# Performance work log

Measured on AMD Instinct MI355X. Metric: run time of the kernel, lower is better.

## Reference

```python
import jax, jax.numpy as jnp
import numpy as np

B, C, H, W = 4, 256, 64, 64
DQK = C // 8  # 32
EPS = 1e-5

def conv1x1(x, Wt, b):
    # 1x1 conv == per-pixel channel matmul. x: [B,C,H,W], Wt: [O,C], b: [O]
    return jnp.einsum('bchw,oc->bohw', x, Wt) + b[None, :, None, None]

def setup_inputs() -> dict:
    key = jax.random.key(0)
    ks = jax.random.split(key, 4)
    s = 1.0 / np.sqrt(C)
    return {
        'x': jax.random.normal(ks[0], (B, C, H, W), dtype=jnp.float32),
        'Wq': jax.random.normal(ks[1], (DQK, C), dtype=jnp.float32) * s,
        'bq': jnp.zeros((DQK,), dtype=jnp.float32),
        'Wk': jax.random.normal(ks[2], (DQK, C), dtype=jnp.float32) * s,
        'bk': jnp.zeros((DQK,), dtype=jnp.float32),
        'Wv': jax.random.normal(ks[3], (C, C), dtype=jnp.float32) * s,
        'bv': jnp.zeros((C,), dtype=jnp.float32),
        'bn_gamma': jnp.ones((C,), dtype=jnp.float32),
        'bn_beta': jnp.zeros((C,), dtype=jnp.float32),
    }

def reference(x, Wq, bq, Wk, bk, Wv, bv, bn_gamma, bn_beta):
    b, c, h, w = x.shape
    n = h * w
    q = conv1x1(x, Wq, bq).reshape(b, -1, n)   # [B, C/8, N]
    k = conv1x1(x, Wk, bk).reshape(b, -1, n)   # [B, C/8, N]
    v = conv1x1(x, Wv, bv).reshape(b, -1, n)   # [B, C,   N]
    # attention_weights = softmax(Q^T K) over last dim (no 1/sqrt(d) scaling)
    attn = jax.nn.softmax(jnp.einsum('bdi,bdj->bij', q, k), axis=-1)  # [B,N,N]
    out = jnp.einsum('bci,bij->bcj', v, attn).reshape(b, c, h, w)
    # BatchNorm2d (training mode: batch stats over B,H,W, biased var)
    mean = jnp.mean(out, axis=(0, 2, 3), keepdims=True)
    var = jnp.var(out, axis=(0, 2, 3), keepdims=True)
    out = (out - mean) * jax.lax.rsqrt(var + EPS)
    out = out * bn_gamma[None, :, None, None] + bn_beta[None, :, None, None]
    return x + out * 1e-05
```

## Files before the change

### kernel.cpp

```cpp
#include <hip/hip_runtime.h>
#include <hip/hip_bf16.h>

#define NB 4
#define NC 256
#define NN 4096

typedef __bf16 bf16x8 __attribute__((ext_vector_type(8)));
typedef float f32x4 __attribute__((ext_vector_type(4)));
typedef unsigned short u16x4 __attribute__((ext_vector_type(4)));
typedef unsigned short u16x8 __attribute__((ext_vector_type(8)));
typedef unsigned int u32x4 __attribute__((ext_vector_type(4)));

__device__ __forceinline__ unsigned short f2bf(float f) {
  union { float f; unsigned u; } v; v.f = f;
  unsigned r = v.u + 0x7fffu + ((v.u >> 16) & 1u);
  return (unsigned short)(r >> 16);
}
__device__ __forceinline__ float bf2f(unsigned short h) {
  union { unsigned u; float f; } v; v.u = ((unsigned)h) << 16;
  return v.f;
}

__global__ __launch_bounds__(256) void k0_prep(const float* __restrict__ Wq,
                                               const float* __restrict__ Wk,
                                               const float* __restrict__ Wv,
                                               unsigned short* __restrict__ Wcat,
                                               unsigned short* __restrict__ Wvb,
                                               float* __restrict__ stats) {
  int tid = blockIdx.x * 256 + threadIdx.x;
  int nt = gridDim.x * 256;
  for (int i = tid; i < 64 * NC; i += nt) {
    int d = i >> 8, c = i & 255;
    float v = (d < 32) ? Wq[d * NC + c] : Wk[(d - 32) * NC + c];
    Wcat[i] = f2bf(v);
  }
  for (int i = tid; i < NC * NC; i += nt) Wvb[i] = f2bf(Wv[i]);
  for (int i = tid; i < 1024; i += nt) stats[i] = 0.f;
}

__global__ __launch_bounds__(256) void k1_cvt_tr(const float* __restrict__ x,
                                                 unsigned short* __restrict__ xbf,
                                                 unsigned short* __restrict__ xT) {
  __shared__ __align__(16) unsigned short lt[64][68];
  int bid = blockIdx.x;
  int b  = bid >> 8;
  int cb = (bid >> 6) & 3;
  int nb = bid & 63;
  int c0 = cb * 64, n0 = nb * 64;
  int t = threadIdx.x;
  int tc = t >> 4;
  int tn = (t & 15) * 4;
#pragma unroll
  for (int it = 0; it < 4; ++it) {
    int c = c0 + tc + it * 16;
    f32x4 xv = *reinterpret_cast<const f32x4*>(&x[((size_t)b * NC + c) * NN + n0 + tn]);
    u16x4 hv;
    hv[0] = f2bf(xv[0]); hv[1] = f2bf(xv[1]); hv[2] = f2bf(xv[2]); hv[3] = f2bf(xv[3]);
    *reinterpret_cast<u16x4*>(&xbf[((size_t)b * NC + c) * NN + n0 + tn]) = hv;
    *reinterpret_cast<u16x4*>(&lt[tc + it * 16][tn]) = hv;
  }
  __syncthreads();
  int nl = t >> 2;
  int cl0 = (t & 3) * 16;
  u16x8 o0, o1;
#pragma unroll
  for (int q = 0; q < 8; ++q) o0[q] = lt[cl0 + q][nl];
#pragma unroll
  for (int q = 0; q < 8; ++q) o1[q] = lt[cl0 + 8 + q][nl];
  size_t ro = ((size_t)b * NN + n0 + nl) * NC + c0 + cl0;
  *reinterpret_cast<u16x8*>(&xT[ro]) = o0;
  *reinterpret_cast<u16x8*>(&xT[ro + 8]) = o1;
}

__global__ __launch_bounds__(256, 2) void k2_qk(const unsigned short* __restrict__ xT,
                                                const unsigned short* __restrict__ Wcat,
                                                const float* __restrict__ bq,
                                                const float* __restrict__ bk,
                                                unsigned short* __restrict__ Qt,
                                                unsigned short* __restrict__ Kt) {
  __shared__ __align__(16) unsigned short lt2[64][72];
  int bid = blockIdx.x;
  int b = bid >> 6, it = bid & 63;
  int i0 = it * 64;
  int t = threadIdx.x;
  int w = t >> 6, l = t & 63, l15 = l & 15, g = l >> 4;

  f32x4 acc[4];
#pragma unroll
  for (int f = 0; f < 4; ++f) acc[f] = f32x4{0.f, 0.f, 0.f, 0.f};

  const unsigned short* xrow = &xT[((size_t)b * NN + i0 + w * 16 + l15) * NC];
#pragma unroll
  for (int ks = 0; ks < 8; ++ks) {
    bf16x8 a = *reinterpret_cast<const bf16x8*>(&xrow[ks * 32 + g * 8]);
#pragma unroll
    for (int f = 0; f < 4; ++f) {
      bf16x8 bb = *reinterpret_cast<const bf16x8*>(&Wcat[(f * 16 + l15) * NC + ks * 32 + g * 8]);
      acc[f] = __builtin_amdgcn_mfma_f32_16x16x32_bf16(a, bb, acc[f], 0, 0, 0);
    }
  }
#pragma unroll
  for (int f = 0; f < 4; ++f) {
    int d = f * 16 + l15;
    float bias = (f < 2) ? bq[d] : bk[d - 32];
#pragma unroll
    for (int r = 0; r < 4; ++r)
      lt2[w * 16 + g * 4 + r][d] = f2bf(acc[f][r] + bias);
  }
  __syncthreads();
  int il = t >> 2, quad = t & 3;
  u32x4 v0 = *reinterpret_cast<const u32x4*>(&lt2[il][quad * 16]);
  u32x4 v1 = *reinterpret_cast<const u32x4*>(&lt2[il][quad * 16 + 8]);
  unsigned short* dst = (quad < 2) ? &Qt[((size_t)b * NN + i0 + il) * 32 + quad * 16]
                                   : &Kt[((size_t)b * NN + i0 + il) * 32 + (quad - 2) * 16];
  *reinterpret_cast<u32x4*>(dst) = v0;
  *reinterpret_cast<u32x4*>(&dst[8]) = v1;
}

__global__ __launch_bounds__(256, 4) void k3_rowsum(const unsigned short* __restrict__ Qt,
                                                    const unsigned short* __restrict__ Kt,
                                                    float* __restrict__ invD) {
  __shared__ float sred[4][16];
  int bid = blockIdx.x;
  int b = bid >> 8, it = bid & 255;
  int i0 = it * 16;
  int t = threadIdx.x, w = t >> 6, l = t & 63, l15 = l & 15, g = l >> 4;
  bf16x8 a = *reinterpret_cast<const bf16x8*>(&Qt[((size_t)b * NN + i0 + l15) * 32 + g * 8]);
  float rs0 = 0.f, rs1 = 0.f, rs2 = 0.f, rs3 = 0.f;
  int jbase = w * 1024;
  for (int jc = 0; jc < 16; ++jc) {
    int jb = jbase + jc * 64;
#pragma unroll
    for (int f = 0; f < 4; ++f) {
      bf16x8 bb = *reinterpret_cast<const bf16x8*>(&Kt[((size_t)b * NN + jb + f * 16 + l15) * 32 + g * 8]);
      f32x4 s = __builtin_amdgcn_mfma_f32_16x16x32_bf16(a, bb, f32x4{0.f, 0.f, 0.f, 0.f}, 0, 0, 0);
      rs0 += __expf(s[0]); rs1 += __expf(s[1]); rs2 += __expf(s[2]); rs3 += __expf(s[3]);
    }
  }
#pragma unroll
  for (int m = 1; m < 16; m <<= 1) {
    rs0 += __shfl_xor(rs0, m); rs1 += __shfl_xor(rs1, m);
    rs2 += __shfl_xor(rs2, m); rs3 += __shfl_xor(rs3, m);
  }
  if (l15 == 0) {
    sred[w][g * 4 + 0] = rs0; sred[w][g * 4 + 1] = rs1;
    sred[w][g * 4 + 2] = rs2; sred[w][g * 4 + 3] = rs3;
  }
  __syncthreads();
  if (t < 16) {
    float d = sred[0][t] + sred[1][t] + sred[2][t] + sred[3][t];
    invD[(size_t)b * NN + i0 + t] = 1.0f / d;
  }
}

__global__ __launch_bounds__(256, 2) void k4_attn(const unsigned short* __restrict__ xbf,
                                                  const unsigned short* __restrict__ Qt,
                                                  const unsigned short* __restrict__ Kt,
                                                  const float* __restrict__ invD,
                                                  unsigned short* __restrict__ TtL,
                                                  unsigned short* __restrict__ TtH,
                                                  float* __restrict__ sLo,
                                                  float* __restrict__ sHi) {
  __shared__ __align__(16) unsigned short plt[4096];
  __shared__ float sArr[4][64];
  int bid = blockIdx.x;
  int b = bid >> 7, ih = (bid >> 6) & 1, jt = bid & 63;
  int j0 = jt * 64;
  int t = threadIdx.x, w = t >> 6, l = t & 63, l15 = l & 15, g = l >> 4;
  unsigned short* Tt = ih ? TtH : TtL;
  float* scol = ih ? sHi : sLo;

  bf16x8 bkf[4];
#pragma unroll
  for (int f = 0; f < 4; ++f)
    bkf[f] = *reinterpret_cast<const bf16x8*>(&Kt[((size_t)b * NN + j0 + f * 16 + l15) * 32 + g * 8]);

  f32x4 acc[4][4];
#pragma unroll
  for (int ci = 0; ci < 4; ++ci)
#pragma unroll
    for (int f = 0; f < 4; ++f) acc[ci][f] = f32x4{0.f, 0.f, 0.f, 0.f};
  float scs[4] = {0.f, 0.f, 0.f, 0.f};

  for (int ic = 0; ic < 32; ++ic) {
    int ibase = (ih * 32 + ic) * 64;
    bf16x8 aq = *reinterpret_cast<const bf16x8*>(&Qt[((size_t)b * NN + ibase + w * 16 + l15) * 32 + g * 8]);
    f32x4 inv4 = *reinterpret_cast<const f32x4*>(&invD[(size_t)b * NN + ibase + w * 16 + g * 4]);
#pragma unroll
    for (int f = 0; f < 4; ++f) {
      f32x4 s = __builtin_amdgcn_mfma_f32_16x16x32_bf16(aq, bkf[f], f32x4{0.f, 0.f, 0.f, 0.f}, 0, 0, 0);
      float p0 = __expf(s[0]) * inv4[0];
      float p1 = __expf(s[1]) * inv4[1];
      float p2 = __expf(s[2]) * inv4[2];
      float p3 = __expf(s[3]) * inv4[3];
      scs[f] += (p0 + p1) + (p2 + p3);
      int j = f * 16 + l15;
      int u = (2 * w + (g >> 1)) ^ (j & 7);
      int idx = j * 64 + u * 8 + (g & 1) * 4;
      u16x4 pk;
      pk[0] = f2bf(p0); pk[1] = f2bf(p1); pk[2] = f2bf(p2); pk[3] = f2bf(p3);
      *reinterpret_cast<u16x4*>(&plt[idx]) = pk;
    }
    __syncthreads();
#pragma unroll
    for (int kb = 0; kb < 2; ++kb) {
      bf16x8 ax[4];
#pragma unroll
      for (int ci = 0; ci < 4; ++ci)
        ax[ci] = *reinterpret_cast<const bf16x8*>(
            &xbf[((size_t)b * NC + w * 64 + ci * 16 + l15) * NN + ibase + kb * 32 + g * 8]);
      bf16x8 bp[4];
#pragma unroll
      for (int f = 0; f < 4; ++f) {
        int j = f * 16 + l15;
        int u = (4 * kb + g) ^ (j & 7);
        bp[f] = *reinterpret_cast<const bf16x8*>(&plt[j * 64 + u * 8]);
      }
#pragma unroll
      for (int ci = 0; ci < 4; ++ci)
#pragma unroll
        for (int f = 0; f < 4; ++f)
          acc[ci][f] = __builtin_amdgcn_mfma_f32_16x16x32_bf16(ax[ci], bp[f], acc[ci][f], 0, 0, 0);
    }
    __syncthreads();
  }
#pragma unroll
  for (int f = 0; f < 4; ++f) {
    scs[f] += __shfl_xor(scs[f], 16);
    scs[f] += __shfl_xor(scs[f], 32);
  }
  if (l < 16) {
#pragma unroll
    for (int f = 0; f < 4; ++f) sArr[w][f * 16 + l] = scs[f];
  }
  __syncthreads();
  if (t < 64) scol[(size_t)b * NN + j0 + t] = sArr[0][t] + sArr[1][t] + sArr[2][t] + sArr[3][t];
#pragma unroll
  for (int ci = 0; ci < 4; ++ci)
#pragma unroll
    for (int f = 0; f < 4; ++f) {
      u16x4 pk;
      pk[0] = f2bf(acc[ci][f][0]); pk[1] = f2bf(acc[ci][f][1]);
      pk[2] = f2bf(acc[ci][f][2]); pk[3] = f2bf(acc[ci][f][3]);
      *reinterpret_cast<u16x4*>(
          &Tt[((size_t)b * NN + j0 + f * 16 + l15) * NC + w * 64 + ci * 16 + g * 4]) = pk;
    }
}

__global__ __launch_bounds__(256, 2) void k5_out(const unsigned short* __restrict__ Wvb,
                                                 const unsigned short* __restrict__ TtL,
                                                 const unsigned short* __restrict__ TtH,
                                                 const float* __restrict__ sLo,
                                                 const float* __restrict__ sHi,
                                                 const float* __restrict__ bv,
                                                 unsigned short* __restrict__ outbf,
                                                 float* __restrict__ stats) {
  int bid = blockIdx.x;
  int b = bid >> 6, jt = bid & 63;
  int j0 = jt * 64;
  int t = threadIdx.x, w = t >> 6, l = t & 63, l15 = l & 15, g = l >> 4;
  f32x4 acc[4][4];
#pragma unroll
  for (int ci = 0; ci < 4; ++ci)
#pragma unroll
    for (int f = 0; f < 4; ++f) acc[ci][f] = f32x4{0.f, 0.f, 0.f, 0.f};

#pragma unroll
  for (int h = 0; h < 2; ++h) {
    const unsigned short* T = h ? TtH : TtL;
#pragma unroll
    for (int ks = 0; ks < 8; ++ks) {
      bf16x8 a[4], bb[4];
#pragma unroll
      for (int ci = 0; ci < 4; ++ci)
        a[ci] = *reinterpret_cast<const bf16x8*>(&Wvb[(w * 64 + ci * 16 + l15) * NC + ks * 32 + g * 8]);
#pragma unroll
      for (int f = 0; f < 4; ++f)
        bb[f] = *reinterpret_cast<const bf16x8*>(&T[((size_t)b * NN + j0 + f * 16 + l15) * NC + ks * 32 + g * 8]);
#pragma unroll
      for (int ci = 0; ci < 4; ++ci)
#pragma unroll
        for (int f = 0; f < 4; ++f)
          acc[ci][f] = __builtin_amdgcn_mfma_f32_16x16x32_bf16(a[ci], bb[f], acc[ci][f], 0, 0, 0);
    }
  }
  float sv[4];
#pragma unroll
  for (int f = 0; f < 4; ++f) {
    size_t ji = (size_t)b * NN + j0 + f * 16 + l15;
    sv[f] = sLo[ji] + sHi[ji];
  }
#pragma unroll
  for (int ci = 0; ci < 4; ++ci) {
    f32x4 bv4 = *reinterpret_cast<const f32x4*>(&bv[w * 64 + ci * 16 + g * 4]);
#pragma unroll
    for (int r = 0; r < 4; ++r) {
      int c = w * 64 + ci * 16 + g * 4 + r;
      float vsum = 0.f, vsq = 0.f;
#pragma unroll
      for (int f = 0; f < 4; ++f) {
        float v = acc[ci][f][r] + bv4[r] * sv[f];
        outbf[((size_t)b * NC + c) * NN + j0 + f * 16 + l15] = f2bf(v);
        vsum += v; vsq += v * v;
      }
#pragma unroll
      for (int m = 1; m < 16; m <<= 1) { vsum += __shfl_xor(vsum, m); vsq += __shfl_xor(vsq, m); }
      if (l15 == 0) { atomicAdd(&stats[c], vsum); atomicAdd(&stats[256 + c], vsq); }
    }
  }
}

__global__ __launch_bounds__(256) void k6_fin(const float* __restrict__ gamma,
                                              const float* __restrict__ beta,
                                              float* __restrict__ stats) {
  int c = threadIdx.x;
  float mean = stats[c] * (1.0f / 16384.0f);
  float var = stats[256 + c] * (1.0f / 16384.0f) - mean * mean;
  float rstd = rsqrtf(var + 1e-5f);
  float sc = gamma[c] * rstd;
  stats[512 + c] = sc * 1e-5f;
  stats[768 + c] = (beta[c] - mean * sc) * 1e-5f;
}

__global__ __launch_bounds__(256) void k7_final(const float* __restrict__ x,
                                                const unsigned short* __restrict__ outbf,
                                                const float* __restrict__ stats,
                                                float* __restrict__ y) {
  int tid = blockIdx.x * 256 + threadIdx.x;
  size_t base = (size_t)tid * 8;
  int c = (int)((base >> 12) & 255);
  float sc = stats[512 + c], sh = stats[768 + c];
  u16x8 ov = *reinterpret_cast<const u16x8*>(&outbf[base]);
  f32x4 x0 = *reinterpret_cast<const f32x4*>(&x[base]);
  f32x4 x1 = *reinterpret_cast<const f32x4*>(&x[base + 4]);
  f32x4 y0, y1;
#pragma unroll
  for (int q = 0; q < 4; ++q) y0[q] = x0[q] + bf2f(ov[q]) * sc + sh;
#pragma unroll
  for (int q = 0; q < 4; ++q) y1[q] = x1[q] + bf2f(ov[4 + q]) * sc + sh;
  *reinterpret_cast<f32x4*>(&y[base]) = y0;
  *reinterpret_cast<f32x4*>(&y[base + 4]) = y1;
}

extern "C" void kernel_launch(void* const* d_in, const int* in_sizes, int n_in,
                              void* d_out, int out_size, void* d_ws, size_t ws_size,
                              hipStream_t stream) {
  (void)in_sizes; (void)n_in; (void)out_size;
  if (ws_size < 27627520) return;

  const float* x    = (const float*)d_in[0];
  const float* Wq   = (const float*)d_in[1];
  const float* bq   = (const float*)d_in[2];
  const float* Wk   = (const float*)d_in[3];
  const float* bk   = (const float*)d_in[4];
  const float* Wv   = (const float*)d_in[5];
  const float* bv   = (const float*)d_in[6];
  const float* gam  = (const float*)d_in[7];
  const float* bet  = (const float*)d_in[8];
  float* y = (float*)d_out;
  char* ws = (char*)d_ws;

  unsigned short* xbf  = (unsigned short*)(ws + 0);
  unsigned short* xT   = (unsigned short*)(ws + 8388608);
  unsigned short* Qt   = (unsigned short*)(ws + 16777216);
  unsigned short* Kt   = (unsigned short*)(ws + 17825792);
  float* invD          = (float*)(ws + 18874368);
  unsigned short* TtH  = (unsigned short*)(ws + 18939904);
  float* sLo           = (float*)(ws + 27328512);
  float* sHi           = (float*)(ws + 27394048);
  float* stats         = (float*)(ws + 27459584);
  unsigned short* Wcat = (unsigned short*)(ws + 27463680);
  unsigned short* Wvb  = (unsigned short*)(ws + 27496448);
  unsigned short* TtL  = xT;
  unsigned short* outbf = xbf;

  hipLaunchKernelGGL(k0_prep,  dim3(256),  dim3(256), 0, stream, Wq, Wk, Wv, Wcat, Wvb, stats);
  hipLaunchKernelGGL(k1_cvt_tr,dim3(1024), dim3(256), 0, stream, x, xbf, xT);
  hipLaunchKernelGGL(k2_qk,    dim3(256),  dim3(256), 0, stream, xT, Wcat, bq, bk, Qt, Kt);
  hipLaunchKernelGGL(k3_rowsum,dim3(1024), dim3(256), 0, stream, Qt, Kt, invD);
  hipLaunchKernelGGL(k4_attn,  dim3(512),  dim3(256), 0, stream, xbf, Qt, Kt, invD, TtL, TtH, sLo, sHi);
  hipLaunchKernelGGL(k5_out,   dim3(256),  dim3(256), 0, stream, Wvb, TtL, TtH, sLo, sHi, bv, outbf, stats);
  hipLaunchKernelGGL(k6_fin,   dim3(1),    dim3(256), 0, stream, gam, bet, stats);
  hipLaunchKernelGGL(k7_final, dim3(2048), dim3(256), 0, stream, x, outbf, stats, y);
}
```

Before: 250.5 us.

## Halve attention j-tile, double-buffer P in LDS, prefetch, exp2 and split stats kernel

The attention kernel now uses 32-column j tiles with 1024 blocks and higher occupancy. It double-buffers the P tile in shared memory to drop one barrier per iteration, and prefetches the x, Q and invD loads for the next chunk. LOG2E is folded into Q so exp2 replaces expf, bf16 conversion uses the hardware cast, and buffer layouts are unified. The BN statistics move out of k5's per-element atomics into a separate reduction kernel over outbf. This costs an extra launch and an extra read pass, and the stats are now computed from bf16-rounded values.

```diff
diff --git a/kernel.cpp b/kernel.cpp
--- a/kernel.cpp
+++ b/kernel.cpp
@@ -11,10 +11,18 @@
 typedef unsigned short u16x8 __attribute__((ext_vector_type(8)));
 typedef unsigned int u32x4 __attribute__((ext_vector_type(4)));
 
+#if __has_builtin(__builtin_amdgcn_exp2f)
+#define EXP2(x) __builtin_amdgcn_exp2f(x)
+#else
+#define EXP2(x) exp2f(x)
+#endif
+
+#define LOG2E 1.4426950408889634f
+
 __device__ __forceinline__ unsigned short f2bf(float f) {
-  union { float f; unsigned u; } v; v.f = f;
-  unsigned r = v.u + 0x7fffu + ((v.u >> 16) & 1u);
-  return (unsigned short)(r >> 16);
+  union { __bf16 h; unsigned short u; } v;
+  v.h = (__bf16)f;
+  return v.u;
 }
 __device__ __forceinline__ float bf2f(unsigned short h) {
   union { unsigned u; float f; } v; v.u = ((unsigned)h) << 16;
@@ -103,9 +111,10 @@
   for (int f = 0; f < 4; ++f) {
     int d = f * 16 + l15;
     float bias = (f < 2) ? bq[d] : bk[d - 32];
+    float scale = (f < 2) ? LOG2E : 1.0f;
 #pragma unroll
     for (int r = 0; r < 4; ++r)
-      lt2[w * 16 + g * 4 + r][d] = f2bf(acc[f][r] + bias);
+      lt2[w * 16 + g * 4 + r][d] = f2bf((acc[f][r] + bias) * scale);
   }
   __syncthreads();
   int il = t >> 2, quad = t & 3;
@@ -134,7 +143,7 @@
     for (int f = 0; f < 4; ++f) {
       bf16x8 bb = *reinterpret_cast<const bf16x8*>(&Kt[((size_t)b * NN + jb + f * 16 + l15) * 32 + g * 8]);
       f32x4 s = __builtin_amdgcn_mfma_f32_16x16x32_bf16(a, bb, f32x4{0.f, 0.f, 0.f, 0.f}, 0, 0, 0);
-      rs0 += __expf(s[0]); rs1 += __expf(s[1]); rs2 += __expf(s[2]); rs3 += __expf(s[3]);
+      rs0 += EXP2(s[0]); rs1 += EXP2(s[1]); rs2 += EXP2(s[2]); rs3 += EXP2(s[3]);
     }
   }
 #pragma unroll
@@ -153,142 +162,150 @@
   }
 }
 
-__global__ __launch_bounds__(256, 2) void k4_attn(const unsigned short* __restrict__ xbf,
+__global__ __launch_bounds__(256, 4) void k4_attn(const unsigned short* __restrict__ xbf,
                                                   const unsigned short* __restrict__ Qt,
                                                   const unsigned short* __restrict__ Kt,
                                                   const float* __restrict__ invD,
-                                                  unsigned short* __restrict__ TtL,
-                                                  unsigned short* __restrict__ TtH,
-                                                  float* __restrict__ sLo,
-                                                  float* __restrict__ sHi) {
-  __shared__ __align__(16) unsigned short plt[4096];
-  __shared__ float sArr[4][64];
+                                                  unsigned short* __restrict__ Tt,
+                                                  float* __restrict__ scol) {
+  __shared__ __align__(16) unsigned short plt[2][2048];
+  __shared__ float sArr[4][32];
   int bid = blockIdx.x;
-  int b = bid >> 7, ih = (bid >> 6) & 1, jt = bid & 63;
-  int j0 = jt * 64;
+  int jt = bid & 127;
+  int ih = (bid >> 7) & 1;
+  int b  = bid >> 8;
+  int j0 = jt * 32;
   int t = threadIdx.x, w = t >> 6, l = t & 63, l15 = l & 15, g = l >> 4;
-  unsigned short* Tt = ih ? TtH : TtL;
-  float* scol = ih ? sHi : sLo;
-
-  bf16x8 bkf[4];
-#pragma unroll
-  for (int f = 0; f < 4; ++f)
-    bkf[f] = *reinterpret_cast<const bf16x8*>(&Kt[((size_t)b * NN + j0 + f * 16 + l15) * 32 + g * 8]);
-
-  f32x4 acc[4][4];
+  unsigned short* Tt_p = Tt + (size_t)ih * ((size_t)NB * NN * NC);
+  float* scol_p = scol + (size_t)ih * (NB * NN);
+  int i0base = ih * 2048;
+  const size_t qbase = (size_t)b * NN;
+
+  bf16x8 bkf[2];
+#pragma unroll
+  for (int f = 0; f < 2; ++f)
+    bkf[f] = *reinterpret_cast<const bf16x8*>(&Kt[(qbase + j0 + f * 16 + l15) * 32 + g * 8]);
+
+  f32x4 acc[4][2];
 #pragma unroll
   for (int ci = 0; ci < 4; ++ci)
 #pragma unroll
-    for (int f = 0; f < 4; ++f) acc[ci][f] = f32x4{0.f, 0.f, 0.f, 0.f};
-  float scs[4] = {0.f, 0.f, 0.f, 0.f};
+    for (int f = 0; f < 2; ++f) acc[ci][f] = f32x4{0.f, 0.f, 0.f, 0.f};
+  float scs[2] = {0.f, 0.f};
+
+  bf16x8 aq = *reinterpret_cast<const bf16x8*>(&Qt[(qbase + i0base + w * 16 + l15) * 32 + g * 8]);
+  f32x4 inv4 = *reinterpret_cast<const f32x4*>(&invD[qbase + i0base + w * 16 + g * 4]);
+  int buf = 0;
 
   for (int ic = 0; ic < 32; ++ic) {
-    int ibase = (ih * 32 + ic) * 64;
-    bf16x8 aq = *reinterpret_cast<const bf16x8*>(&Qt[((size_t)b * NN + ibase + w * 16 + l15) * 32 + g * 8]);
-    f32x4 inv4 = *reinterpret_cast<const f32x4*>(&invD[(size_t)b * NN + ibase + w * 16 + g * 4]);
-#pragma unroll
-    for (int f = 0; f < 4; ++f) {
+    int ibase = i0base + ic * 64;
+    unsigned short* pb = plt[buf];
+#pragma unroll
+    for (int f = 0; f < 2; ++f) {
       f32x4 s = __builtin_amdgcn_mfma_f32_16x16x32_bf16(aq, bkf[f], f32x4{0.f, 0.f, 0.f, 0.f}, 0, 0, 0);
-      float p0 = __expf(s[0]) * inv4[0];
-      float p1 = __expf(s[1]) * inv4[1];
-      float p2 = __expf(s[2]) * inv4[2];
-      float p3 = __expf(s[3]) * inv4[3];
+      float p0 = EXP2(s[0]) * inv4[0];
+      float p1 = EXP2(s[1]) * inv4[1];
+      float p2 = EXP2(s[2]) * inv4[2];
+      float p3 = EXP2(s[3]) * inv4[3];
       scs[f] += (p0 + p1) + (p2 + p3);
       int j = f * 16 + l15;
       int u = (2 * w + (g >> 1)) ^ (j & 7);
-      int idx = j * 64 + u * 8 + (g & 1) * 4;
       u16x4 pk;
       pk[0] = f2bf(p0); pk[1] = f2bf(p1); pk[2] = f2bf(p2); pk[3] = f2bf(p3);
-      *reinterpret_cast<u16x4*>(&plt[idx]) = pk;
+      *reinterpret_cast<u16x4*>(&pb[j * 64 + u * 8 + (g & 1) * 4]) = pk;
+    }
+    bf16x8 axr[2][4];
+#pragma unroll
+    for (int kb = 0; kb < 2; ++kb)
+#pragma unroll
+      for (int ci = 0; ci < 4; ++ci)
+        axr[kb][ci] = *reinterpret_cast<const bf16x8*>(
+            &xbf[((size_t)b * NC + w * 64 + ci * 16 + l15) * NN + ibase + kb * 32 + g * 8]);
+    if (ic + 1 < 32) {
+      aq = *reinterpret_cast<const bf16x8*>(&Qt[(qbase + ibase + 64 + w * 16 + l15) * 32 + g * 8]);
+      inv4 = *reinterpret_cast<const f32x4*>(&invD[qbase + ibase + 64 + w * 16 + g * 4]);
     }
     __syncthreads();
 #pragma unroll
     for (int kb = 0; kb < 2; ++kb) {
-      bf16x8 ax[4];
-#pragma unroll
-      for (int ci = 0; ci < 4; ++ci)
-        ax[ci] = *reinterpret_cast<const bf16x8*>(
-            &xbf[((size_t)b * NC + w * 64 + ci * 16 + l15) * NN + ibase + kb * 32 + g * 8]);
-      bf16x8 bp[4];
-#pragma unroll
-      for (int f = 0; f < 4; ++f) {
+      bf16x8 bp[2];
+#pragma unroll
+      for (int f = 0; f < 2; ++f) {
         int j = f * 16 + l15;
-        int u = (4 * kb + g) ^ (j & 7);
-        bp[f] = *reinterpret_cast<const bf16x8*>(&plt[j * 64 + u * 8]);
+        int u = (kb * 4 + g) ^ (j & 7);
+        bp[f] = *reinterpret_cast<const bf16x8*>(&pb[j * 64 + u * 8]);
       }
 #pragma unroll
-      for (int ci = 0; ci < 4; ++ci)
-#pragma unroll
-        for (int f = 0; f < 4; ++f)
-          acc[ci][f] = __builtin_amdgcn_mfma_f32_16x16x32_bf16(ax[ci], bp[f], acc[ci][f], 0, 0, 0);
-    }
-    __syncthreads();
-  }
-#pragma unroll
-  for (int f = 0; f < 4; ++f) {
+      for (int ci = 0; ci < 4; ++ci) {
+        acc[ci][0] = __builtin_amdgcn_mfma_f32_16x16x32_bf16(axr[kb][ci], bp[0], acc[ci][0], 0, 0, 0);
+        acc[ci][1] = __builtin_amdgcn_mfma_f32_16x16x32_bf16(axr[kb][ci], bp[1], acc[ci][1], 0, 0, 0);
+      }
+    }
+    buf ^= 1;
+  }
+#pragma unroll
+  for (int f = 0; f < 2; ++f) {
     scs[f] += __shfl_xor(scs[f], 16);
     scs[f] += __shfl_xor(scs[f], 32);
   }
   if (l < 16) {
-#pragma unroll
-    for (int f = 0; f < 4; ++f) sArr[w][f * 16 + l] = scs[f];
+    sArr[w][l] = scs[0];
+    sArr[w][16 + l] = scs[1];
   }
   __syncthreads();
-  if (t < 64) scol[(size_t)b * NN + j0 + t] = sArr[0][t] + sArr[1][t] + sArr[2][t] + sArr[3][t];
+  if (t < 32) scol_p[qbase + j0 + t] = sArr[0][t] + sArr[1][t] + sArr[2][t] + sArr[3][t];
 #pragma unroll
   for (int ci = 0; ci < 4; ++ci)
 #pragma unroll
-    for (int f = 0; f < 4; ++f) {
+    for (int f = 0; f < 2; ++f) {
       u16x4 pk;
       pk[0] = f2bf(acc[ci][f][0]); pk[1] = f2bf(acc[ci][f][1]);
       pk[2] = f2bf(acc[ci][f][2]); pk[3] = f2bf(acc[ci][f][3]);
       *reinterpret_cast<u16x4*>(
-          &Tt[((size_t)b * NN + j0 + f * 16 + l15) * NC + w * 64 + ci * 16 + g * 4]) = pk;
+          &Tt_p[(qbase + j0 + f * 16 + l15) * NC + w * 64 + ci * 16 + g * 4]) = pk;
     }
 }
 
 __global__ __launch_bounds__(256, 2) void k5_out(const unsigned short* __restrict__ Wvb,
-                                                 const unsigned short* __restrict__ TtL,
-                                                 const unsigned short* __restrict__ TtH,
-                                                 const float* __restrict__ sLo,
-                                                 const float* __restrict__ sHi,
+                                                 const unsigned short* __restrict__ Tt,
+                                                 const float* __restrict__ scol,
                                                  const float* __restrict__ bv,
-                                                 unsigned short* __restrict__ outbf,
-                                                 float* __restrict__ stats) {
+                                                 unsigned short* __restrict__ outbf) {
   int bid = blockIdx.x;
-  int b = bid >> 6, jt = bid & 63;
-  int j0 = jt * 64;
+  int b = bid >> 7, jt = bid & 127;
+  int j0 = jt * 32;
   int t = threadIdx.x, w = t >> 6, l = t & 63, l15 = l & 15, g = l >> 4;
-  f32x4 acc[4][4];
+  f32x4 acc[4][2];
 #pragma unroll
   for (int ci = 0; ci < 4; ++ci)
 #pragma unroll
-    for (int f = 0; f < 4; ++f) acc[ci][f] = f32x4{0.f, 0.f, 0.f, 0.f};
-
-#pragma unroll
-  for (int h = 0; h < 2; ++h) {
-    const unsigned short* T = h ? TtH : TtL;
-#pragma unroll
-    for (int ks = 0; ks < 8; ++ks) {
-      bf16x8 a[4], bb[4];
-#pragma unroll
-      for (int ci = 0; ci < 4; ++ci)
-        a[ci] = *reinterpret_cast<const bf16x8*>(&Wvb[(w * 64 + ci * 16 + l15) * NC + ks * 32 + g * 8]);
-#pragma unroll
-      for (int f = 0; f < 4; ++f)
+    for (int f = 0; f < 2; ++f) acc[ci][f] = f32x4{0.f, 0.f, 0.f, 0.f};
+
+#pragma unroll
+  for (int ks = 0; ks < 8; ++ks) {
+    bf16x8 a[4];
+#pragma unroll
+    for (int ci = 0; ci < 4; ++ci)
+      a[ci] = *reinterpret_cast<const bf16x8*>(&Wvb[(w * 64 + ci * 16 + l15) * NC + ks * 32 + g * 8]);
+#pragma unroll
+    for (int h = 0; h < 2; ++h) {
+      const unsigned short* T = Tt + (size_t)h * ((size_t)NB * NN * NC);
+      bf16x8 bb[2];
+#pragma unroll
+      for (int f = 0; f < 2; ++f)
         bb[f] = *reinterpret_cast<const bf16x8*>(&T[((size_t)b * NN + j0 + f * 16 + l15) * NC + ks * 32 + g * 8]);
 #pragma unroll
-      for (int ci = 0; ci < 4; ++ci)
-#pragma unroll
-        for (int f = 0; f < 4; ++f)
-          acc[ci][f] = __builtin_amdgcn_mfma_f32_16x16x32_bf16(a[ci], bb[f], acc[ci][f], 0, 0, 0);
-    }
-  }
-  float sv[4];
-#pragma unroll
-  for (int f = 0; f < 4; ++f) {
+      for (int ci = 0; ci < 4; ++ci) {
+        acc[ci][0] = __builtin_amdgcn_mfma_f32_16x16x32_bf16(a[ci], bb[0], acc[ci][0], 0, 0, 0);
+        acc[ci][1] = __builtin_amdgcn_mfma_f32_16x16x32_bf16(a[ci], bb[1], acc[ci][1], 0, 0, 0);
+      }
+    }
+  }
+  float sv[2];
+#pragma unroll
+  for (int f = 0; f < 2; ++f) {
     size_t ji = (size_t)b * NN + j0 + f * 16 + l15;
-    sv[f] = sLo[ji] + sHi[ji];
+    sv[f] = scol[ji] + scol[(size_t)NB * NN + ji];
   }
 #pragma unroll
   for (int ci = 0; ci < 4; ++ci) {
@@ -296,17 +313,38 @@
 #pragma unroll
     for (int r = 0; r < 4; ++r) {
       int c = w * 64 + ci * 16 + g * 4 + r;
-      float vsum = 0.f, vsq = 0.f;
-#pragma unroll
-      for (int f = 0; f < 4; ++f) {
-        float v = acc[ci][f][r] + bv4[r] * sv[f];
-        outbf[((size_t)b * NC + c) * NN + j0 + f * 16 + l15] = f2bf(v);
-        vsum += v; vsq += v * v;
-      }
-#pragma unroll
-      for (int m = 1; m < 16; m <<= 1) { vsum += __shfl_xor(vsum, m); vsq += __shfl_xor(vsq, m); }
-      if (l15 == 0) { atomicAdd(&stats[c], vsum); atomicAdd(&stats[256 + c], vsq); }
-    }
+#pragma unroll
+      for (int f = 0; f < 2; ++f)
+        outbf[((size_t)b * NC + c) * NN + j0 + f * 16 + l15] = f2bf(acc[ci][f][r] + bv4[r] * sv[f]);
+    }
+  }
+}
+
+__global__ __launch_bounds__(256) void k5a_stats(const unsigned short* __restrict__ outbf,
+                                                 float* __restrict__ stats) {
+  __shared__ float sred[2][4];
+  int c = blockIdx.x >> 1, half = blockIdx.x & 1;
+  int t = threadIdx.x;
+  float sum = 0.f, sq = 0.f;
+#pragma unroll
+  for (int b = 0; b < 4; ++b) {
+    u16x8 v = *reinterpret_cast<const u16x8*>(
+        &outbf[((((size_t)b << 8) + c) << 12) + half * 2048 + t * 8]);
+#pragma unroll
+    for (int q = 0; q < 8; ++q) {
+      float f = bf2f(v[q]);
+      sum += f; sq = fmaf(f, f, sq);
+    }
+  }
+#pragma unroll
+  for (int m = 1; m < 64; m <<= 1) {
+    sum += __shfl_xor(sum, m); sq += __shfl_xor(sq, m);
+  }
+  if ((t & 63) == 0) { sred[0][t >> 6] = sum; sred[1][t >> 6] = sq; }
+  __syncthreads();
+  if (t == 0) {
+    atomicAdd(&stats[c],       sred[0][0] + sred[0][1] + sred[0][2] + sred[0][3]);
+    atomicAdd(&stats[256 + c], sred[1][0] + sred[1][1] + sred[1][2] + sred[1][3]);
   }
 }
 
@@ -361,25 +399,24 @@
   char* ws = (char*)d_ws;
 
   unsigned short* xbf  = (unsigned short*)(ws + 0);
-  unsigned short* xT   = (unsigned short*)(ws + 8388608);
-  unsigned short* Qt   = (unsigned short*)(ws + 16777216);
-  unsigned short* Kt   = (unsigned short*)(ws + 17825792);
-  float* invD          = (float*)(ws + 18874368);
-  unsigned short* TtH  = (unsigned short*)(ws + 18939904);
-  float* sLo           = (float*)(ws + 27328512);
-  float* sHi           = (float*)(ws + 27394048);
+  unsigned short* Tt   = (unsigned short*)(ws + 8388608);
+  unsigned short* Qt   = (unsigned short*)(ws + 25165824);
+  unsigned short* Kt   = (unsigned short*)(ws + 26214400);
+  float* invD          = (float*)(ws + 27262976);
+  float* scol          = (float*)(ws + 27328512);
   float* stats         = (float*)(ws + 27459584);
   unsigned short* Wcat = (unsigned short*)(ws + 27463680);
   unsigned short* Wvb  = (unsigned short*)(ws + 27496448);
-  unsigned short* TtL  = xT;
+  unsigned short* xT   = Tt;
   unsigned short* outbf = xbf;
 
   hipLaunchKernelGGL(k0_prep,  dim3(256),  dim3(256), 0, stream, Wq, Wk, Wv, Wcat, Wvb, stats);
   hipLaunchKernelGGL(k1_cvt_tr,dim3(1024), dim3(256), 0, stream, x, xbf, xT);
   hipLaunchKernelGGL(k2_qk,    dim3(256),  dim3(256), 0, stream, xT, Wcat, bq, bk, Qt, Kt);
   hipLaunchKernelGGL(k3_rowsum,dim3(1024), dim3(256), 0, stream, Qt, Kt, invD);
-  hipLaunchKernelGGL(k4_attn,  dim3(512),  dim3(256), 0, stream, xbf, Qt, Kt, invD, TtL, TtH, sLo, sHi);
-  hipLaunchKernelGGL(k5_out,   dim3(256),  dim3(256), 0, stream, Wvb, TtL, TtH, sLo, sHi, bv, outbf, stats);
+  hipLaunchKernelGGL(k4_attn,  dim3(1024), dim3(256), 0, stream, xbf, Qt, Kt, invD, Tt, scol);
+  hipLaunchKernelGGL(k5_out,   dim3(512),  dim3(256), 0, stream, Wvb, Tt, scol, bv, outbf);
+  hipLaunchKernelGGL(k5a_stats,dim3(512),  dim3(256), 0, stream, outbf, stats);
   hipLaunchKernelGGL(k6_fin,   dim3(1),    dim3(256), 0, stream, gam, bet, stats);
   hipLaunchKernelGGL(k7_final, dim3(2048), dim3(256), 0, stream, x, outbf, stats, y);
 }
```

Measured after the change: 268.5 us. 7.2% more time.
